# Performance work log

Measured on AMD Instinct MI355X. Metric: run time of the kernel, lower is better.

The kernel has to match this reference:

```python
import jax, jax.numpy as jnp
import numpy as np

LEAKY_SLOPE = 0.01  # torch F.leaky_relu default
LN_EPS = 1e-5       # torch nn.LayerNorm default


def _layer_norm(x, g, b):
    mu = jnp.mean(x, axis=-1, keepdims=True)
    var = jnp.var(x, axis=-1, keepdims=True)
    return (x - mu) * jax.lax.rsqrt(var + LN_EPS) * g + b


def _gcn(x, adj, W, b):
    # GraphConvolution (Kipf-style): adj @ (x @ W) + b
    return adj @ (x @ W) + b


def setup_inputs() -> dict:
    key = jax.random.key(0)
    ks = jax.random.split(key, 8)
    N, fan_in, fan_mid, fan_out = 12288, 128, 128, 20
    h0, h1, h2 = fan_mid, fan_mid // 2, fan_mid // 4  # 128, 64, 32
    inp = {
        "x": jax.random.normal(ks[0], (N, fan_in), dtype=jnp.float32),
        "adj0": jax.random.uniform(ks[1], (N, N), dtype=jnp.float32),
        "adj1": jax.random.uniform(ks[2], (N, N), dtype=jnp.float32),
        "adj2": jax.random.uniform(ks[3], (N, N), dtype=jnp.float32),
        "W0": jax.random.normal(ks[4], (fan_in, h0), dtype=jnp.float32) / np.sqrt(fan_in),
        "b0": jnp.zeros((h0,), dtype=jnp.float32),
        "W1": jax.random.normal(ks[5], (h0, h1), dtype=jnp.float32) / np.sqrt(h0),
        "b1": jnp.zeros((h1,), dtype=jnp.float32),
        "W2": jax.random.normal(ks[6], (h1, h2), dtype=jnp.float32) / np.sqrt(h1),
        "b2": jnp.zeros((h2,), dtype=jnp.float32),
        "g0": jnp.ones((h0,), dtype=jnp.float32),
        "be0": jnp.zeros((h0,), dtype=jnp.float32),
        "g1": jnp.ones((h1,), dtype=jnp.float32),
        "be1": jnp.zeros((h1,), dtype=jnp.float32),
        "g2": jnp.ones((h2,), dtype=jnp.float32),
        "be2": jnp.zeros((h2,), dtype=jnp.float32),
        "Wl": jax.random.normal(ks[7], (h2, fan_out), dtype=jnp.float32) / np.sqrt(h2),
        "bl": jnp.zeros((fan_out,), dtype=jnp.float32),
    }
    return inp


def reference(x, adj0, adj1, adj2, W0, b0, W1, b1, W2, b2,
              g0, be0, g1, be1, g2, be2, Wl, bl):
    # first GCN + LayerNorm (no activation, matching the original forward)
    h = _layer_norm(_gcn(x, adj0, W0, b0), g0, be0)
    # two loop iterations: GCN -> LN -> LeakyReLU -> Dropout(eval=identity)
    h = jax.nn.leaky_relu(_layer_norm(_gcn(h, adj1, W1, b1), g1, be1), LEAKY_SLOPE)
    h = jax.nn.leaky_relu(_layer_norm(_gcn(h, adj2, W2, b2), g2, be2), LEAKY_SLOPE)
    logits = h @ Wl + bl
    return jax.nn.log_softmax(logits, axis=1)
```

## Files before the change

kernel.cpp:

```cpp
#include <hip/hip_runtime.h>
#include <cstdint>
#include <cstddef>

typedef __attribute__((ext_vector_type(8))) short short8;
typedef __attribute__((ext_vector_type(4))) float f32x4;

#define DEV __device__ __forceinline__

DEV unsigned short f2bf(float f) {
  unsigned int u = __float_as_uint(f);
  u += 0x7fffu + ((u >> 16) & 1u);
  return (unsigned short)(u >> 16);
}

DEV unsigned int pk2(float a, float b) {
  return (unsigned int)f2bf(a) | ((unsigned int)f2bf(b) << 16);
}

DEV void glds16(const void* g, void* l) {
  __builtin_amdgcn_global_load_lds(
      (const __attribute__((address_space(1))) void*)g,
      (__attribute__((address_space(3))) void*)l, 16, 0, 0);
}

constexpr int NROW = 12288;

__global__ __launch_bounds__(256) void xw_kernel(
    const float* __restrict__ x, const float* __restrict__ W0,
    unsigned short* __restrict__ t0T) {
  __shared__ float sW[128 * 128];
  __shared__ float sx[16][128];
  const int t = threadIdx.x;
  for (int i = t; i < 128 * 128; i += 256) sW[i] = W0[i];
  const int r0 = blockIdx.x * 16;
  for (int i = t; i < 16 * 128; i += 256)
    sx[i >> 7][i & 127] = x[(size_t)(r0 + (i >> 7)) * 128 + (i & 127)];
  __syncthreads();
  const int c = t & 127;
  const int rg = t >> 7;
  float acc[8] = {0, 0, 0, 0, 0, 0, 0, 0};
  for (int k = 0; k < 128; ++k) {
    float w = sW[k * 128 + c];
#pragma unroll
    for (int j = 0; j < 8; ++j) acc[j] += sx[rg * 8 + j][k] * w;
  }
  uint4 o;
  o.x = pk2(acc[0], acc[1]);
  o.y = pk2(acc[2], acc[3]);
  o.z = pk2(acc[4], acc[5]);
  o.w = pk2(acc[6], acc[7]);
  *(uint4*)(t0T + (size_t)c * NROW + r0 + rg * 8) = o;
}

template <int H>
__global__ __launch_bounds__(256, 3) void gcn_gemm(
    const float* __restrict__ A, const unsigned short* __restrict__ BT,
    float* __restrict__ part) {
  constexpr int KSPLIT = 4;
  constexpr int BM = 64, BK = 64;
  constexpr int WN = (H >= 64) ? 2 : 1;
  constexpr int WM = 4 / WN;
  constexpr int MR = BM / (WM * 16);
  constexpr int NR = H / (WN * 16);
  constexpr int NB = H / 32;
  constexpr int KSTEPS = (NROW / KSPLIT) / BK;
  constexpr int NSUP = KSTEPS / 3;
  constexpr int BBYTES = H * 128;
  static_assert(KSTEPS % 3 == 0, "");

  __shared__ alignas(16) char lds[16384 + 2 * BBYTES];
  char* ldsB = lds + 16384;

  const int t = threadIdx.x;
  const int xcd = blockIdx.x & 7;
  const int idx = blockIdx.x >> 3;
  const int split = xcd >> 1;
  const int bm = ((xcd & 1) ? 96 : 0) + idx;
  const int k0 = split * (NROW / KSPLIT);

  const int r = t >> 2, q = t & 3;
  const float* aptr = A + (size_t)(bm * BM + r) * NROW + k0 + q * 16;
  const int sw = (r & 7) << 4;
  const int aw0 = (r * 128 + q * 32) ^ sw;
  const int aw1 = (r * 128 + q * 32 + 16) ^ sw;

  const int nB0 = t >> 3;
  const int wB = (t & 7) ^ (nB0 & 7);
  const unsigned short* bptr = BT + (size_t)nB0 * NROW + k0 + wB * 8;
  const int wid = t >> 6;
  char* ldsBw = ldsB + wid * 1024;

  const int lane = t & 63;
  const int l15 = lane & 15;
  const int loct = lane >> 4;
  const int wm = wid / WN;
  const int wn = wid % WN;
  int aoff[MR][2], boff[NR][2];
#pragma unroll
  for (int m = 0; m < MR; ++m)
#pragma unroll
    for (int kk = 0; kk < 2; ++kk) {
      int row = wm * (MR * 16) + m * 16 + l15;
      aoff[m][kk] = (row * 128 + kk * 64 + loct * 16) ^ ((row & 7) << 4);
    }
#pragma unroll
  for (int n = 0; n < NR; ++n)
#pragma unroll
    for (int kk = 0; kk < 2; ++kk) {
      int nn = wn * (NR * 16) + n * 16 + l15;
      boff[n][kk] = (nn * 128 + kk * 64 + loct * 16) ^ ((nn & 7) << 4);
    }

  f32x4 acc[MR][NR];
#pragma unroll
  for (int m = 0; m < MR; ++m)
#pragma unroll
    for (int n = 0; n < NR; ++n) acc[m][n] = {0.f, 0.f, 0.f, 0.f};

  float4 av[12];

  auto issueSuper = [&](int S) {
#pragma unroll
    for (int j = 0; j < 3; ++j)
#pragma unroll
      for (int i = 0; i < 4; ++i)
        av[j * 4 + i] = *(const float4*)(aptr + S * 192 + j * 64 + i * 4);
  };
  auto glB = [&](int s, int buf) {
#pragma unroll
    for (int j = 0; j < NB; ++j)
      glds16(bptr + (size_t)j * 32 * NROW + s * BK,
             ldsBw + buf * BBYTES + j * 4096);
  };
  auto cvtWrite = [&](int j, int buf) {
    char* wb = lds + buf * 8192;
    uint4 w0, w1;
    w0.x = pk2(av[j * 4 + 0].x, av[j * 4 + 0].y);
    w0.y = pk2(av[j * 4 + 0].z, av[j * 4 + 0].w);
    w0.z = pk2(av[j * 4 + 1].x, av[j * 4 + 1].y);
    w0.w = pk2(av[j * 4 + 1].z, av[j * 4 + 1].w);
    w1.x = pk2(av[j * 4 + 2].x, av[j * 4 + 2].y);
    w1.y = pk2(av[j * 4 + 2].z, av[j * 4 + 2].w);
    w1.z = pk2(av[j * 4 + 3].x, av[j * 4 + 3].y);
    w1.w = pk2(av[j * 4 + 3].z, av[j * 4 + 3].w);
    *(uint4*)(wb + aw0) = w0;
    *(uint4*)(wb + aw1) = w1;
  };
  auto compute = [&](int buf) {
    const char* lA = lds + buf * 8192;
    const char* lB = ldsB + buf * BBYTES;
#pragma unroll
    for (int kk = 0; kk < 2; ++kk) {
      short8 af[MR], bfv[NR];
#pragma unroll
      for (int m = 0; m < MR; ++m) af[m] = *(const short8*)(lA + aoff[m][kk]);
#pragma unroll
      for (int n = 0; n < NR; ++n) bfv[n] = *(const short8*)(lB + boff[n][kk]);
#pragma unroll
      for (int m = 0; m < MR; ++m)
#pragma unroll
        for (int n = 0; n < NR; ++n)
          acc[m][n] = __builtin_amdgcn_mfma_f32_16x16x32_bf16(
              af[m], bfv[n], acc[m][n], 0, 0, 0);
    }
  };

  issueSuper(0);
  glB(0, 0);
  cvtWrite(0, 0);
  asm volatile("s_waitcnt vmcnt(0) lgkmcnt(0)" ::: "memory");
  __builtin_amdgcn_s_barrier();
  __builtin_amdgcn_sched_barrier(0);

  for (int S = 0; S < NSUP; ++S) {
    const int b = S & 1;
    glB(3 * S + 1, b ^ 1);
    compute(b);
    cvtWrite(1, b ^ 1);
    asm volatile("s_waitcnt vmcnt(0) lgkmcnt(0)" ::: "memory");
    __builtin_amdgcn_s_barrier();
    __builtin_amdgcn_sched_barrier(0);
    glB(3 * S + 2, b);
    compute(b ^ 1);
    cvtWrite(2, b);
    if (S + 1 < NSUP) {
      issueSuper(S + 1);
      asm volatile("s_waitcnt vmcnt(12) lgkmcnt(0)" ::: "memory");
    } else {
      asm volatile("s_waitcnt vmcnt(0) lgkmcnt(0)" ::: "memory");
    }
    __builtin_amdgcn_s_barrier();
    __builtin_amdgcn_sched_barrier(0);
    if (S + 1 < NSUP) {
      glB(3 * S + 3, b ^ 1);
      compute(b);
      cvtWrite(0, b ^ 1);
      asm volatile("s_waitcnt vmcnt(0) lgkmcnt(0)" ::: "memory");
      __builtin_amdgcn_s_barrier();
      __builtin_amdgcn_sched_barrier(0);
    } else {
      compute(b);
    }
  }

  float* pout = part + ((size_t)split * NROW + (size_t)bm * BM) * H;
#pragma unroll
  for (int m = 0; m < MR; ++m) {
    const int row = wm * (MR * 16) + m * 16 + loct * 4;
#pragma unroll
    for (int n = 0; n < NR; ++n) {
      const int col = wn * (NR * 16) + n * 16 + l15;
#pragma unroll
      for (int rr = 0; rr < 4; ++rr)
        pout[(size_t)(row + rr) * H + col] = acc[m][n][rr];
    }
  }
}

template <int H, int H2, bool ACT>
__global__ __launch_bounds__(256) void reduce_ln(
    const float* __restrict__ part, const float* __restrict__ bias,
    const float* __restrict__ g, const float* __restrict__ be,
    const float* __restrict__ Wn, unsigned short* __restrict__ tT) {
  __shared__ float sW[H * H2];
  __shared__ float sh[4][H];
  const int t = threadIdx.x;
  for (int i = t; i < H * H2; i += 256) sW[i] = Wn[i];
  __syncthreads();

  const int wid = t >> 6, lane = t & 63;
  const int row = blockIdx.x * 4 + wid;
  constexpr int CPL = H / 64;
  float v[CPL];
#pragma unroll
  for (int c = 0; c < CPL; ++c) {
    const int col = lane + c * 64;
    float s = bias[col];
#pragma unroll
    for (int sp = 0; sp < 4; ++sp)
      s += part[((size_t)sp * NROW + row) * H + col];
    v[c] = s;
  }
  float sum = 0;
#pragma unroll
  for (int c = 0; c < CPL; ++c) sum += v[c];
#pragma unroll
  for (int o = 32; o > 0; o >>= 1) sum += __shfl_xor(sum, o);
  const float mu = sum / H;
  float vs = 0;
#pragma unroll
  for (int c = 0; c < CPL; ++c) { float d = v[c] - mu; vs += d * d; }
#pragma unroll
  for (int o = 32; o > 0; o >>= 1) vs += __shfl_xor(vs, o);
  const float rstd = rsqrtf(vs / H + 1e-5f);
#pragma unroll
  for (int c = 0; c < CPL; ++c) {
    const int col = lane + c * 64;
    float h = (v[c] - mu) * rstd * g[col] + be[col];
    if (ACT) h = (h > 0.f) ? h : 0.01f * h;
    sh[wid][col] = h;
  }
  __syncthreads();
  if (lane < H2) {
    float d = 0;
#pragma unroll 8
    for (int k = 0; k < H; ++k) d += sh[wid][k] * sW[k * H2 + lane];
    tT[(size_t)lane * NROW + row] = f2bf(d);
  }
}

__global__ __launch_bounds__(256) void reduce_final(
    const float* __restrict__ part, const float* __restrict__ bias,
    const float* __restrict__ g, const float* __restrict__ be,
    const float* __restrict__ Wl, const float* __restrict__ bl,
    float* __restrict__ out) {
  __shared__ float sW[32 * 20];
  __shared__ float sbl[20];
  __shared__ float sh[4][32];
  __shared__ float sl[4][20];
  const int t = threadIdx.x;
  for (int i = t; i < 640; i += 256) sW[i] = Wl[i];
  if (t < 20) sbl[t] = bl[t];
  __syncthreads();
  const int wid = t >> 6, lane = t & 63;
  const int row = blockIdx.x * 4 + wid;
  const int col = lane & 31;
  float v = bias[col];
#pragma unroll
  for (int sp = 0; sp < 4; ++sp)
    v += part[((size_t)sp * NROW + row) * 32 + col];
  float sum = v;
#pragma unroll
  for (int o = 32; o > 0; o >>= 1) sum += __shfl_xor(sum, o);
  const float mu = sum / 64.f;
  float d0 = v - mu;
  float vs = d0 * d0;
#pragma unroll
  for (int o = 32; o > 0; o >>= 1) vs += __shfl_xor(vs, o);
  const float rstd = rsqrtf(vs / 64.f + 1e-5f);
  float h = (v - mu) * rstd * g[col] + be[col];
  h = (h > 0.f) ? h : 0.01f * h;
  if (lane < 32) sh[wid][col] = h;
  __syncthreads();
  if (lane < 20) {
    float lg = sbl[lane];
#pragma unroll
    for (int k = 0; k < 32; ++k) lg += sh[wid][k] * sW[k * 20 + lane];
    sl[wid][lane] = lg;
  }
  __syncthreads();
  if (lane < 20) {
    float mx = -1e30f;
#pragma unroll
    for (int k = 0; k < 20; ++k) mx = fmaxf(mx, sl[wid][k]);
    float se = 0.f;
#pragma unroll
    for (int k = 0; k < 20; ++k) se += expf(sl[wid][k] - mx);
    out[(size_t)row * 20 + lane] = sl[wid][lane] - mx - logf(se);
  }
}

extern "C" void kernel_launch(void* const* d_in, const int* in_sizes, int n_in,
                              void* d_out, int out_size, void* d_ws,
                              size_t ws_size, hipStream_t stream) {
  const float* x    = (const float*)d_in[0];
  const float* adj0 = (const float*)d_in[1];
  const float* adj1 = (const float*)d_in[2];
  const float* adj2 = (const float*)d_in[3];
  const float* W0   = (const float*)d_in[4];
  const float* b0   = (const float*)d_in[5];
  const float* W1   = (const float*)d_in[6];
  const float* b1   = (const float*)d_in[7];
  const float* W2   = (const float*)d_in[8];
  const float* b2   = (const float*)d_in[9];
  const float* g0   = (const float*)d_in[10];
  const float* be0  = (const float*)d_in[11];
  const float* g1   = (const float*)d_in[12];
  const float* be1  = (const float*)d_in[13];
  const float* g2   = (const float*)d_in[14];
  const float* be2  = (const float*)d_in[15];
  const float* Wl   = (const float*)d_in[16];
  const float* bl   = (const float*)d_in[17];
  float* out = (float*)d_out;

  char* ws = (char*)d_ws;
  float* part =          (float*)(ws);
  unsigned short* t0T = (unsigned short*)(ws + 25165824);
  unsigned short* t1T = (unsigned short*)(ws + 25165824 + 3145728);
  unsigned short* t2T = (unsigned short*)(ws + 25165824 + 3145728 + 1572864);

  xw_kernel<<<NROW / 16, 256, 0, stream>>>(x, W0, t0T);
  gcn_gemm<128><<<(NROW / 64) * 4, 256, 0, stream>>>(adj0, t0T, part);
  reduce_ln<128, 64, false><<<NROW / 4, 256, 0, stream>>>(part, b0, g0, be0, W1, t1T);
  gcn_gemm<64><<<(NROW / 64) * 4, 256, 0, stream>>>(adj1, t1T, part);
  reduce_ln<64, 32, true><<<NROW / 4, 256, 0, stream>>>(part, b1, g1, be1, W2, t2T);
  gcn_gemm<32><<<(NROW / 64) * 4, 256, 0, stream>>>(adj2, t2T, part);
  reduce_final<<<NROW / 4, 256, 0, stream>>>(part, b2, g2, be2, Wl, bl, out);
}
```

Before: 457.4 us.

## Load fp32 adjacency directly into MFMA registers, bypassing LDS staging

Each wave now owns 16 rows of the 64-row A tile and loads its MFMA A-fragment straight from global memory into registers. It converts to bf16 in registers just before the MFMA, so the A tile is no longer written to LDS and read back, and LDS use drops to the B double buffer. The k-loop becomes a two-step register double-buffered pipeline with waitcnt-controlled prefetch, replacing the three-step super-iteration. In exchange, each lane's global A reads are 32-byte fragments at a row stride, which may coalesce worse than the previous row-contiguous pattern, and every wave now reads the whole B tile.

```diff
diff --git a/kernel.cpp b/kernel.cpp
--- a/kernel.cpp
+++ b/kernel.cpp
@@ -58,18 +58,13 @@
     float* __restrict__ part) {
   constexpr int KSPLIT = 4;
   constexpr int BM = 64, BK = 64;
-  constexpr int WN = (H >= 64) ? 2 : 1;
-  constexpr int WM = 4 / WN;
-  constexpr int MR = BM / (WM * 16);
-  constexpr int NR = H / (WN * 16);
+  constexpr int NR = H / 16;
   constexpr int NB = H / 32;
   constexpr int KSTEPS = (NROW / KSPLIT) / BK;
-  constexpr int NSUP = KSTEPS / 3;
   constexpr int BBYTES = H * 128;
-  static_assert(KSTEPS % 3 == 0, "");
-
-  __shared__ alignas(16) char lds[16384 + 2 * BBYTES];
-  char* ldsB = lds + 16384;
+  static_assert((KSTEPS & 1) == 0, "");
+
+  __shared__ alignas(16) char ldsB[2 * BBYTES];
 
   const int t = threadIdx.x;
   const int xcd = blockIdx.x & 7;
@@ -78,53 +73,38 @@
   const int bm = ((xcd & 1) ? 96 : 0) + idx;
   const int k0 = split * (NROW / KSPLIT);
 
-  const int r = t >> 2, q = t & 3;
-  const float* aptr = A + (size_t)(bm * BM + r) * NROW + k0 + q * 16;
-  const int sw = (r & 7) << 4;
-  const int aw0 = (r * 128 + q * 32) ^ sw;
-  const int aw1 = (r * 128 + q * 32 + 16) ^ sw;
+  const int wid = t >> 6, lane = t & 63;
+  const int l15 = lane & 15, loct = lane >> 4;
+
+  const float* aptr =
+      A + (size_t)(bm * BM + wid * 16 + l15) * NROW + k0 + loct * 8;
 
   const int nB0 = t >> 3;
   const int wB = (t & 7) ^ (nB0 & 7);
   const unsigned short* bptr = BT + (size_t)nB0 * NROW + k0 + wB * 8;
-  const int wid = t >> 6;
   char* ldsBw = ldsB + wid * 1024;
 
-  const int lane = t & 63;
-  const int l15 = lane & 15;
-  const int loct = lane >> 4;
-  const int wm = wid / WN;
-  const int wn = wid % WN;
-  int aoff[MR][2], boff[NR][2];
-#pragma unroll
-  for (int m = 0; m < MR; ++m)
+  int boff[NR][2];
+#pragma unroll
+  for (int n = 0; n < NR; ++n)
 #pragma unroll
     for (int kk = 0; kk < 2; ++kk) {
-      int row = wm * (MR * 16) + m * 16 + l15;
-      aoff[m][kk] = (row * 128 + kk * 64 + loct * 16) ^ ((row & 7) << 4);
-    }
-#pragma unroll
-  for (int n = 0; n < NR; ++n)
-#pragma unroll
-    for (int kk = 0; kk < 2; ++kk) {
-      int nn = wn * (NR * 16) + n * 16 + l15;
+      int nn = n * 16 + l15;
       boff[n][kk] = (nn * 128 + kk * 64 + loct * 16) ^ ((nn & 7) << 4);
     }
 
-  f32x4 acc[MR][NR];
-#pragma unroll
-  for (int m = 0; m < MR; ++m)
-#pragma unroll
-    for (int n = 0; n < NR; ++n) acc[m][n] = {0.f, 0.f, 0.f, 0.f};
-
-  float4 av[12];
-
-  auto issueSuper = [&](int S) {
-#pragma unroll
-    for (int j = 0; j < 3; ++j)
-#pragma unroll
-      for (int i = 0; i < 4; ++i)
-        av[j * 4 + i] = *(const float4*)(aptr + S * 192 + j * 64 + i * 4);
+  f32x4 acc[NR];
+#pragma unroll
+  for (int n = 0; n < NR; ++n) acc[n] = {0.f, 0.f, 0.f, 0.f};
+
+  f32x4 arA[4], arB[4];
+
+  auto issueA = [&](f32x4* ar, int s) {
+#pragma unroll
+    for (int kk = 0; kk < 2; ++kk)
+#pragma unroll
+      for (int h = 0; h < 2; ++h)
+        ar[kk * 2 + h] = *(const f32x4*)(aptr + s * BK + kk * 32 + h * 4);
   };
   auto glB = [&](int s, int buf) {
 #pragma unroll
@@ -132,89 +112,64 @@
       glds16(bptr + (size_t)j * 32 * NROW + s * BK,
              ldsBw + buf * BBYTES + j * 4096);
   };
-  auto cvtWrite = [&](int j, int buf) {
-    char* wb = lds + buf * 8192;
-    uint4 w0, w1;
-    w0.x = pk2(av[j * 4 + 0].x, av[j * 4 + 0].y);
-    w0.y = pk2(av[j * 4 + 0].z, av[j * 4 + 0].w);
-    w0.z = pk2(av[j * 4 + 1].x, av[j * 4 + 1].y);
-    w0.w = pk2(av[j * 4 + 1].z, av[j * 4 + 1].w);
-    w1.x = pk2(av[j * 4 + 2].x, av[j * 4 + 2].y);
-    w1.y = pk2(av[j * 4 + 2].z, av[j * 4 + 2].w);
-    w1.z = pk2(av[j * 4 + 3].x, av[j * 4 + 3].y);
-    w1.w = pk2(av[j * 4 + 3].z, av[j * 4 + 3].w);
-    *(uint4*)(wb + aw0) = w0;
-    *(uint4*)(wb + aw1) = w1;
-  };
-  auto compute = [&](int buf) {
-    const char* lA = lds + buf * 8192;
+  auto compute = [&](const f32x4* ar, int buf) {
     const char* lB = ldsB + buf * BBYTES;
 #pragma unroll
     for (int kk = 0; kk < 2; ++kk) {
-      short8 af[MR], bfv[NR];
-#pragma unroll
-      for (int m = 0; m < MR; ++m) af[m] = *(const short8*)(lA + aoff[m][kk]);
-#pragma unroll
-      for (int n = 0; n < NR; ++n) bfv[n] = *(const short8*)(lB + boff[n][kk]);
-#pragma unroll
-      for (int m = 0; m < MR; ++m)
-#pragma unroll
-        for (int n = 0; n < NR; ++n)
-          acc[m][n] = __builtin_amdgcn_mfma_f32_16x16x32_bf16(
-              af[m], bfv[n], acc[m][n], 0, 0, 0);
+      union { unsigned int u[4]; short8 s8; } afu;
+      afu.u[0] = pk2(ar[kk * 2].x, ar[kk * 2].y);
+      afu.u[1] = pk2(ar[kk * 2].z, ar[kk * 2].w);
+      afu.u[2] = pk2(ar[kk * 2 + 1].x, ar[kk * 2 + 1].y);
+      afu.u[3] = pk2(ar[kk * 2 + 1].z, ar[kk * 2 + 1].w);
+      const short8 af = afu.s8;
+#pragma unroll
+      for (int n = 0; n < NR; ++n) {
+        const short8 bf = *(const short8*)(lB + boff[n][kk]);
+        acc[n] = __builtin_amdgcn_mfma_f32_16x16x32_bf16(af, bf, acc[n],
+                                                         0, 0, 0);
+      }
     }
   };
 
-  issueSuper(0);
   glB(0, 0);
-  cvtWrite(0, 0);
+  __builtin_amdgcn_sched_barrier(0);
+  issueA(arA, 0);
+  issueA(arB, 1);
+  asm volatile("s_waitcnt vmcnt(4)" ::: "memory");
+  __builtin_amdgcn_s_barrier();
+  __builtin_amdgcn_sched_barrier(0);
+
+  for (int s = 0; s < KSTEPS - 2; s += 2) {
+    glB(s + 1, 1);
+    __builtin_amdgcn_sched_barrier(0);
+    compute(arA, 0);
+    issueA(arA, s + 2);
+    asm volatile("s_waitcnt vmcnt(4) lgkmcnt(0)" ::: "memory");
+    __builtin_amdgcn_s_barrier();
+    __builtin_amdgcn_sched_barrier(0);
+    glB(s + 2, 0);
+    __builtin_amdgcn_sched_barrier(0);
+    compute(arB, 1);
+    issueA(arB, s + 3);
+    asm volatile("s_waitcnt vmcnt(4) lgkmcnt(0)" ::: "memory");
+    __builtin_amdgcn_s_barrier();
+    __builtin_amdgcn_sched_barrier(0);
+  }
+
+  glB(KSTEPS - 1, 1);
+  __builtin_amdgcn_sched_barrier(0);
+  compute(arA, 0);
   asm volatile("s_waitcnt vmcnt(0) lgkmcnt(0)" ::: "memory");
   __builtin_amdgcn_s_barrier();
   __builtin_amdgcn_sched_barrier(0);
-
-  for (int S = 0; S < NSUP; ++S) {
-    const int b = S & 1;
-    glB(3 * S + 1, b ^ 1);
-    compute(b);
-    cvtWrite(1, b ^ 1);
-    asm volatile("s_waitcnt vmcnt(0) lgkmcnt(0)" ::: "memory");
-    __builtin_amdgcn_s_barrier();
-    __builtin_amdgcn_sched_barrier(0);
-    glB(3 * S + 2, b);
-    compute(b ^ 1);
-    cvtWrite(2, b);
-    if (S + 1 < NSUP) {
-      issueSuper(S + 1);
-      asm volatile("s_waitcnt vmcnt(12) lgkmcnt(0)" ::: "memory");
-    } else {
-      asm volatile("s_waitcnt vmcnt(0) lgkmcnt(0)" ::: "memory");
-    }
-    __builtin_amdgcn_s_barrier();
-    __builtin_amdgcn_sched_barrier(0);
-    if (S + 1 < NSUP) {
-      glB(3 * S + 3, b ^ 1);
-      compute(b);
-      cvtWrite(0, b ^ 1);
-      asm volatile("s_waitcnt vmcnt(0) lgkmcnt(0)" ::: "memory");
-      __builtin_amdgcn_s_barrier();
-      __builtin_amdgcn_sched_barrier(0);
-    } else {
-      compute(b);
-    }
-  }
-
-  float* pout = part + ((size_t)split * NROW + (size_t)bm * BM) * H;
-#pragma unroll
-  for (int m = 0; m < MR; ++m) {
-    const int row = wm * (MR * 16) + m * 16 + loct * 4;
-#pragma unroll
-    for (int n = 0; n < NR; ++n) {
-      const int col = wn * (NR * 16) + n * 16 + l15;
-#pragma unroll
-      for (int rr = 0; rr < 4; ++rr)
-        pout[(size_t)(row + rr) * H + col] = acc[m][n][rr];
-    }
-  }
+  compute(arB, 1);
+
+  float* pout = part + ((size_t)split * NROW + (size_t)bm * BM + wid * 16) * H;
+#pragma unroll
+  for (int n = 0; n < NR; ++n)
+#pragma unroll
+    for (int rr = 0; rr < 4; ++rr)
+      pout[(size_t)(loct * 4 + rr) * H + n * 16 + l15] = acc[n][rr];
 }
 
 template <int H, int H2, bool ACT>
```

Measured after the change: 481.3 us. 1.05x slower.
